# Kernel tuning notes

Measured on AMD Instinct MI355X. Metric: run time of the kernel, lower is better.

The kernel has to match this reference:

```python
import jax, jax.numpy as jnp
import numpy as np

B = 8192        # batch
F = 16          # num_fields
V = 50000       # vocab per field
D = 32          # embed_dim (all equal per assert)
NE = 3          # number of embedding spaces
NL = 3          # cross-net layers
EOD = F * D     # 512 = embed_output_dim
M1, M2, M3 = 512, 256, 128
REG_WEIGHT = 0.01


def setup_inputs() -> dict:
    key = jax.random.key(0)
    ks = jax.random.split(key, 12)
    x = jax.random.randint(ks[0], (B, F), 0, V)
    emb_tables = jax.random.normal(ks[1], (NE, F * V, D), dtype=jnp.float32) * 0.05
    cross_W = jax.random.normal(ks[2], (NE, NL, EOD, EOD), dtype=jnp.float32) * (1.0 / np.sqrt(EOD))
    cross_b = jnp.zeros((NE, NL, EOD), dtype=jnp.float32)
    mlp1_W = jax.random.normal(ks[3], (NE, EOD, M1), dtype=jnp.float32) * (1.0 / np.sqrt(EOD))
    mlp1_b = jnp.zeros((NE, M1), dtype=jnp.float32)
    mlp_W1 = jax.random.normal(ks[4], (M1, M2), dtype=jnp.float32) * (1.0 / np.sqrt(M1))
    mlp_b1 = jnp.zeros((M2,), dtype=jnp.float32)
    mlp_W2 = jax.random.normal(ks[5], (M2, M3), dtype=jnp.float32) * (1.0 / np.sqrt(M2))
    mlp_b2 = jnp.zeros((M3,), dtype=jnp.float32)
    mlp_W3 = jax.random.normal(ks[6], (M3, 1), dtype=jnp.float32) * (1.0 / np.sqrt(M3))
    mlp_b3 = jnp.zeros((1,), dtype=jnp.float32)
    return {"x": x, "emb_tables": emb_tables, "cross_W": cross_W, "cross_b": cross_b,
            "mlp1_W": mlp1_W, "mlp1_b": mlp1_b, "mlp_W1": mlp_W1, "mlp_b1": mlp_b1,
            "mlp_W2": mlp_W2, "mlp_b2": mlp_b2, "mlp_W3": mlp_W3, "mlp_b3": mlp_b3}


def _branch(x0, Ws, bs, W1, b1):
    # DCNv2 cross network: x_{l+1} = x0 * (W_l x_l + b_l) + x_l, then one MLP layer (ReLU)
    xl = x0
    for l in range(NL):
        xl = x0 * (xl @ Ws[l] + bs[l]) + xl
    return jax.nn.relu(xl @ W1 + b1)


def reference(x, emb_tables, cross_W, cross_b, mlp1_W, mlp1_b,
              mlp_W1, mlp_b1, mlp_W2, mlp_b2, mlp_W3, mlp_b3):
    offsets = jnp.arange(F, dtype=x.dtype) * V
    idx = x + offsets                      # [B, F] indices into shared table
    es = emb_tables[:, idx]                # [NE, B, F, D]
    es_flat = es.reshape(NE, B, EOD)       # [NE, B, F*D]
    h = jax.vmap(_branch)(es_flat, cross_W, cross_b, mlp1_W, mlp1_b)  # [NE, B, M1]
    h = h.mean(axis=0)                     # mean over embedding spaces
    h = jax.nn.relu(h @ mlp_W1 + mlp_b1)
    h = jax.nn.relu(h @ mlp_W2 + mlp_b2)
    p = h @ mlp_W3 + mlp_b3                # [B, 1]
    output = jax.nn.sigmoid(p[:, 0])
    # training-path regularizer: per-field cross-embedding Gram SVDs
    pairs = [(1, 0), (2, 0), (2, 1)]
    sims = []
    for i, j in pairs:
        m = jnp.einsum('bkd,bke->kde', es[i], es[j])     # [F, D, D]
        s = jnp.linalg.svd(m, compute_uv=False)          # batched singular values [F, D]
        sims.append(s.mean(axis=0))                      # [D]
    sim = jnp.concatenate(sims)                          # [len(pairs)*D]
    reg_loss = REG_WEIGHT * jnp.mean(sim ** 2)
    return output, reg_loss
```

## Files before the change

### kernel.cpp

```cpp
#include <hip/hip_runtime.h>
#include <math.h>

#define B_ 8192
#define F_ 16
#define V_ 50000
#define D_ 32
#define NE_ 3
#define EOD_ 512
#define M1_ 512
#define M2_ 256
#define M3_ 128
#define BE_ ((size_t)B_ * EOD_)

typedef __attribute__((ext_vector_type(8))) short short8;
typedef __attribute__((ext_vector_type(4))) float floatx4;

__device__ __forceinline__ unsigned short f2bf(float f) {
    union { float f; unsigned u; } v; v.f = f;
    unsigned r = v.u + 0x7FFF + ((v.u >> 16) & 1);
    return (unsigned short)(r >> 16);
}
__device__ __forceinline__ float bf2f(unsigned short h) {
    union { unsigned u; float f; } v; v.u = (unsigned)h << 16;
    return v.f;
}
__device__ __forceinline__ void gld16(const void* g, void* l) {
    __builtin_amdgcn_global_load_lds(
        (const __attribute__((address_space(1))) unsigned int*)g,
        (__attribute__((address_space(3))) unsigned int*)l, 16, 0, 0);
}

__global__ __launch_bounds__(256) void gather_k(const int* __restrict__ x,
    const float* __restrict__ tables, unsigned short* __restrict__ esb)
{
    int gid = blockIdx.x * 256 + threadIdx.x;
    int d8 = gid & 3;
    int f  = (gid >> 2) & 15;
    int b  = (gid >> 6) & (B_ - 1);
    int e  = gid >> 19;
    int idx = x[b * F_ + f] + f * V_;
    const float4* src = (const float4*)(tables + ((size_t)e * F_ * V_ + idx) * D_) + d8 * 2;
    float4 v0 = src[0], v1 = src[1];
    unsigned short o[8];
    o[0] = f2bf(v0.x); o[1] = f2bf(v0.y); o[2] = f2bf(v0.z); o[3] = f2bf(v0.w);
    o[4] = f2bf(v1.x); o[5] = f2bf(v1.y); o[6] = f2bf(v1.z); o[7] = f2bf(v1.w);
    unsigned short* dst = esb + ((size_t)e * B_ + b) * EOD_ + f * D_ + d8 * 8;
    *(uint4*)dst = *(uint4*)o;
}

__global__ __launch_bounds__(256) void wtrans12_k(const float* __restrict__ crossW,
    const float* __restrict__ mlp1W, unsigned short* __restrict__ Wt)
{
    __shared__ float tile[32][33];
    int bn = blockIdx.x * 32, bk = blockIdx.y * 32;
    int mat = blockIdx.z;
    const float* Wm = (mat < 9) ? crossW + (size_t)mat * 512 * 512
                                : mlp1W + (size_t)(mat - 9) * 512 * 512;
    unsigned short* Wtm = Wt + (size_t)mat * 512 * 512;
    int tx = threadIdx.x & 31, ty = threadIdx.x >> 5;
    #pragma unroll
    for (int i = 0; i < 32; i += 8)
        tile[ty + i][tx] = Wm[(size_t)(bk + ty + i) * 512 + bn + tx];
    __syncthreads();
    #pragma unroll
    for (int i = 0; i < 32; i += 8)
        Wtm[(size_t)(bn + ty + i) * 512 + bk + tx] = f2bf(tile[tx][ty + i]);
}

__global__ __launch_bounds__(256) void wtrans_k(const float* __restrict__ W,
    unsigned short* __restrict__ Wt, int K, int N)
{
    __shared__ float tile[32][33];
    int bn = blockIdx.x * 32, bk = blockIdx.y * 32;
    int tx = threadIdx.x & 31, ty = threadIdx.x >> 5;
    #pragma unroll
    for (int i = 0; i < 32; i += 8)
        tile[ty + i][tx] = W[(size_t)(bk + ty + i) * N + bn + tx];
    __syncthreads();
    #pragma unroll
    for (int i = 0; i < 32; i += 8)
        Wt[(size_t)(bn + ty + i) * K + bk + tx] = f2bf(tile[tx][ty + i]);
}

__global__ __launch_bounds__(256) void gemm_mfma_k(
    const unsigned short* __restrict__ A,  long sA,
    const unsigned short* __restrict__ Wt, long sW,
    const float* __restrict__ bias,        long sB,
    const unsigned short* __restrict__ x0, long sX,
    const unsigned short* __restrict__ xl, long sXl,
    unsigned short* __restrict__ outb,     long sO,
    int M, int N, int K, int mode)
{
    int e = blockIdx.z;
    A    += (size_t)e * sA;
    Wt   += (size_t)e * sW;
    bias += (size_t)e * sB;
    outb += (size_t)e * sO;
    if (mode == 0) { x0 += (size_t)e * sX; xl += (size_t)e * sXl; }

    __shared__ unsigned short As[128 * 32];
    __shared__ unsigned short Bs[128 * 32];
    int t = threadIdx.x;
    int w = t >> 6, lane = t & 63;
    int quad = lane >> 4, lid = lane & 15;
    int wr = (w & 1) * 64, wc = (w >> 1) * 64;
    int rowbase = blockIdx.y * 128, colbase = blockIdx.x * 128;

    int chunk = w * 2;
    int sub = lane >> 2;
    int kk = (lane & 3) * 8;
    const unsigned short* pa0 = A  + (size_t)(rowbase + chunk * 16 + sub) * K + kk;
    const unsigned short* pa1 = pa0 + (size_t)16 * K;
    const unsigned short* pb0 = Wt + (size_t)(colbase + chunk * 16 + sub) * K + kk;
    const unsigned short* pb1 = pb0 + (size_t)16 * K;
    unsigned short* la0 = As + chunk * 512 + lane * 8;
    unsigned short* la1 = la0 + 512;
    unsigned short* lb0 = Bs + chunk * 512 + lane * 8;
    unsigned short* lb1 = lb0 + 512;

    floatx4 acc[4][4];
    #pragma unroll
    for (int i = 0; i < 4; i++)
        #pragma unroll
        for (int j = 0; j < 4; j++) acc[i][j] = {0.f, 0.f, 0.f, 0.f};

    for (int k0 = 0; k0 < K; k0 += 32) {
        if (k0) __syncthreads();
        gld16(pa0 + k0, la0);
        gld16(pa1 + k0, la1);
        gld16(pb0 + k0, lb0);
        gld16(pb1 + k0, lb1);
        __syncthreads();
        short8 af[4], bfr[4];
        #pragma unroll
        for (int i = 0; i < 4; i++) {
            af[i]  = *(const short8*)(As + (wr + i * 16 + lid) * 32 + quad * 8);
            bfr[i] = *(const short8*)(Bs + (wc + i * 16 + lid) * 32 + quad * 8);
        }
        #pragma unroll
        for (int i = 0; i < 4; i++)
            #pragma unroll
            for (int j = 0; j < 4; j++)
                acc[i][j] = __builtin_amdgcn_mfma_f32_16x16x32_bf16(af[i], bfr[j], acc[i][j], 0, 0, 0);
    }

    #pragma unroll
    for (int i = 0; i < 4; i++) {
        int row0 = rowbase + wr + i * 16 + quad * 4;
        #pragma unroll
        for (int j = 0; j < 4; j++) {
            int col = colbase + wc + j * 16 + lid;
            float bv = bias[col];
            #pragma unroll
            for (int rr = 0; rr < 4; rr++) {
                size_t off = (size_t)(row0 + rr) * N + col;
                float v = acc[i][j][rr] + bv;
                if (mode == 0)      v = bf2f(x0[off]) * v + bf2f(xl[off]);
                else if (mode == 1) v = fmaxf(v, 0.f) * (1.f / 3.f);
                else                v = fmaxf(v, 0.f);
                outb[off] = f2bf(v);
            }
        }
    }
}

__global__ __launch_bounds__(256) void sum3_k(const unsigned short* __restrict__ h,
                                              unsigned short* __restrict__ o)
{
    size_t i = ((size_t)blockIdx.x * 256 + threadIdx.x) * 8;
    uint4 a = *(const uint4*)(h + i);
    uint4 b = *(const uint4*)(h + BE_ + i);
    uint4 c = *(const uint4*)(h + 2 * BE_ + i);
    const unsigned short* pa = (const unsigned short*)&a;
    const unsigned short* pb = (const unsigned short*)&b;
    const unsigned short* pc = (const unsigned short*)&c;
    unsigned short r[8];
    #pragma unroll
    for (int j = 0; j < 8; j++) r[j] = f2bf(bf2f(pa[j]) + bf2f(pb[j]) + bf2f(pc[j]));
    *(uint4*)(o + i) = *(uint4*)r;
}

__global__ __launch_bounds__(256) void final_k(const unsigned short* __restrict__ h2,
    const float* __restrict__ W3, const float* __restrict__ b3,
    float* __restrict__ out)
{
    int gt = blockIdx.x * 256 + threadIdx.x;
    int s = gt >> 6, lane = gt & 63;
    float p = bf2f(h2[(size_t)s * 128 + lane]) * W3[lane]
            + bf2f(h2[(size_t)s * 128 + 64 + lane]) * W3[64 + lane];
    #pragma unroll
    for (int off = 32; off > 0; off >>= 1) p += __shfl_down(p, off);
    if (lane == 0) out[s] = 1.0f / (1.0f + expf(-(p + b3[0])));
}

__global__ __launch_bounds__(256) void pairsum_k(const unsigned short* __restrict__ es,
                                                 float* __restrict__ m)
{
    const int pi[3] = {1, 2, 2};
    const int pj[3] = {0, 0, 1};
    int pk = blockIdx.x;
    int pair = pk >> 4, k = pk & 15;
    const unsigned short* Ei = es + (size_t)pi[pair] * BE_ + k * D_;
    const unsigned short* Ej = es + (size_t)pj[pair] * BE_ + k * D_;
    int b0 = blockIdx.y * (B_ / 16);

    __shared__ float sa[8][32], sb[8][32];
    int t = threadIdx.x;
    int d = t >> 3, e4 = (t & 7) * 4;
    int lr = t >> 5, lc = t & 31;
    float a0 = 0, a1 = 0, a2 = 0, a3 = 0;

    for (int bb = b0; bb < b0 + B_ / 16; bb += 8) {
        __syncthreads();
        sa[lr][lc] = bf2f(Ei[(size_t)(bb + lr) * EOD_ + lc]);
        sb[lr][lc] = bf2f(Ej[(size_t)(bb + lr) * EOD_ + lc]);
        __syncthreads();
        #pragma unroll
        for (int s2 = 0; s2 < 8; s2++) {
            float avv = sa[s2][d];
            float4 bvv = *(const float4*)&sb[s2][e4];
            a0 += avv * bvv.x; a1 += avv * bvv.y;
            a2 += avv * bvv.z; a3 += avv * bvv.w;
        }
    }
    float* dst = m + (size_t)pk * 1024 + d * 32 + e4;
    atomicAdd(dst + 0, a0); atomicAdd(dst + 1, a1);
    atomicAdd(dst + 2, a2); atomicAdd(dst + 3, a3);
}

__global__ __launch_bounds__(64) void svd_k(const float* __restrict__ mg,
                                            float* __restrict__ sv)
{
    int mat = blockIdx.x;
    int l = threadIdx.x;
    int col = l & 31, half = l >> 5;
    const float* src = mg + (size_t)mat * 1024 + half * 16 * 32 + col;
    float a[16];
    #pragma unroll
    for (int j = 0; j < 16; j++) a[j] = src[j * 32];

    for (int sweep = 0; sweep < 6; sweep++) {
        for (int r = 0; r < 31; r++) {
            int partner, isp;
            if (col == 31) { partner = r; isp = 1; }
            else {
                int u = col - r; if (u < 0) u += 31;
                if (u == 0) { partner = 31; isp = 0; }
                else {
                    int v = 2 * r - col; v %= 31; if (v < 0) v += 31;
                    partner = v;
                    isp = (u <= 15) ? 1 : 0;
                }
            }
            int plane = half * 32 + partner;
            float b[16];
            #pragma unroll
            for (int j = 0; j < 16; j++) b[j] = __shfl(a[j], plane, 64);
            float own = 0.f, cross = 0.f, par = 0.f;
            #pragma unroll
            for (int j = 0; j < 16; j++) {
                own   += a[j] * a[j];
                cross += a[j] * b[j];
                par   += b[j] * b[j];
            }
            own   += __shfl_xor(own, 32);
            cross += __shfl_xor(cross, 32);
            par   += __shfl_xor(par, 32);
            float app = isp ? own : par;
            float aqq = isp ? par : own;
            float c = 1.f, s = 0.f;
            if (fabsf(cross) > 1e-12f) {
                float tau = (aqq - app) / (2.f * cross);
                float tt = (tau >= 0.f) ? 1.f / (tau + sqrtf(1.f + tau * tau))
                                        : 1.f / (tau - sqrtf(1.f + tau * tau));
                c = rsqrtf(1.f + tt * tt); s = tt * c;
            }
            float sgn = isp ? -s : s;
            #pragma unroll
            for (int j = 0; j < 16; j++) a[j] = c * a[j] + sgn * b[j];
        }
    }

    float nn = 0.f;
    #pragma unroll
    for (int j = 0; j < 16; j++) nn += a[j] * a[j];
    nn += __shfl_xor(nn, 32);
    float v = sqrtf(nn);

    __shared__ float ev[32];
    if (half == 0) ev[col] = v;
    if (half == 0) {
        int rank = 0;
        for (int o2 = 0; o2 < 32; o2++) {
            float w = ev[o2];
            if (w > v || (w == v && o2 < col)) rank++;
        }
        sv[(size_t)mat * 32 + rank] = v;
    }
}

__global__ __launch_bounds__(128) void reg_k(const float* __restrict__ sv,
                                             float* __restrict__ out)
{
    __shared__ float red[128];
    int t = threadIdx.x;
    float val = 0.f;
    if (t < 96) {
        int p = t >> 5, d = t & 31;
        float s = 0;
        #pragma unroll
        for (int k = 0; k < 16; k++) s += sv[(size_t)(p * 16 + k) * 32 + d];
        s *= (1.f / 16.f);
        val = s * s;
    }
    red[t] = val; __syncthreads();
    for (int off = 64; off > 0; off >>= 1) {
        if (t < off) red[t] += red[t + off];
        __syncthreads();
    }
    if (t == 0) out[B_] = 0.01f * red[0] / 96.f;
}

extern "C" void kernel_launch(void* const* d_in, const int* in_sizes, int n_in,
                              void* d_out, int out_size, void* d_ws, size_t ws_size,
                              hipStream_t stream)
{
    const int*   x      = (const int*)d_in[0];
    const float* emb    = (const float*)d_in[1];
    const float* crossW = (const float*)d_in[2];
    const float* crossb = (const float*)d_in[3];
    const float* mlp1W  = (const float*)d_in[4];
    const float* mlp1b  = (const float*)d_in[5];
    const float* W1     = (const float*)d_in[6];
    const float* b1     = (const float*)d_in[7];
    const float* W2     = (const float*)d_in[8];
    const float* b2     = (const float*)d_in[9];
    const float* W3     = (const float*)d_in[10];
    const float* b3     = (const float*)d_in[11];
    float* out = (float*)d_out;

    unsigned char* wsb = (unsigned char*)d_ws;
    size_t o = 0;
    auto alloc = [&](size_t bytes) -> void* {
        void* p = wsb + o; o += (bytes + 255) & ~(size_t)255; return p;
    };
    unsigned short* esb  = (unsigned short*)alloc(3 * BE_ * 2);
    unsigned short* B0   = (unsigned short*)alloc(3 * BE_ * 2);
    unsigned short* B1   = (unsigned short*)alloc(3 * BE_ * 2);
    unsigned short* WtC  = (unsigned short*)alloc((size_t)12 * 512 * 512 * 2);
    unsigned short* Wt1  = (unsigned short*)alloc((size_t)512 * 256 * 2);
    unsigned short* Wt2  = (unsigned short*)alloc((size_t)256 * 128 * 2);
    float*          mbuf = (float*)alloc(48 * 1024 * 4);
    float*          svb  = (float*)alloc(48 * 32 * 4);
    unsigned short* WtM  = WtC + (size_t)9 * 512 * 512;
    unsigned short* hsb = B0;
    unsigned short* h1b = B0 + (size_t)B_ * M1_;
    unsigned short* h2b = h1b + (size_t)B_ * M2_;

    wtrans12_k<<<dim3(16, 16, 12), 256, 0, stream>>>(crossW, mlp1W, WtC);
    wtrans_k<<<dim3( 8, 16), 256, 0, stream>>>(W1, Wt1, 512, 256);
    wtrans_k<<<dim3( 4,  8), 256, 0, stream>>>(W2, Wt2, 256, 128);

    gather_k<<<(NE_ * B_ * F_ * 4) / 256, 256, 0, stream>>>(x, emb, esb);

    hipMemsetAsync(mbuf, 0, 48 * 1024 * 4, stream);
    pairsum_k<<<dim3(48, 16), 256, 0, stream>>>(esb, mbuf);
    svd_k<<<48, 64, 0, stream>>>(mbuf, svb);
    reg_k<<<1, 128, 0, stream>>>(svb, out);

    const long sW512 = 3 * 512 * 512;
    gemm_mfma_k<<<dim3(4, 64, 3), 256, 0, stream>>>(
        esb, (long)BE_, WtC, sW512, crossb, 3 * 512,
        esb, (long)BE_, esb, (long)BE_, B0, (long)BE_, B_, EOD_, EOD_, 0);
    gemm_mfma_k<<<dim3(4, 64, 3), 256, 0, stream>>>(
        B0, (long)BE_, WtC + 512 * 512, sW512, crossb + 512, 3 * 512,
        esb, (long)BE_, B0, (long)BE_, B1, (long)BE_, B_, EOD_, EOD_, 0);
    gemm_mfma_k<<<dim3(4, 64, 3), 256, 0, stream>>>(
        B1, (long)BE_, WtC + 2 * 512 * 512, sW512, crossb + 1024, 3 * 512,
        esb, (long)BE_, B1, (long)BE_, B0, (long)BE_, B_, EOD_, EOD_, 0);
    gemm_mfma_k<<<dim3(4, 64, 3), 256, 0, stream>>>(
        B0, (long)BE_, WtM, 512 * 512, mlp1b, 512,
        nullptr, 0, nullptr, 0, B1, (long)BE_, B_, M1_, EOD_, 1);
    sum3_k<<<(B_ * M1_) / (256 * 8), 256, 0, stream>>>(B1, hsb);
    gemm_mfma_k<<<dim3(2, 64, 1), 256, 0, stream>>>(
        hsb, 0, Wt1, 0, b1, 0, nullptr, 0, nullptr, 0,
        h1b, 0, B_, M2_, M1_, 2);
    gemm_mfma_k<<<dim3(1, 64, 1), 256, 0, stream>>>(
        h1b, 0, Wt2, 0, b2, 0, nullptr, 0, nullptr, 0,
        h2b, 0, B_, M3_, M2_, 2);
    final_k<<<(B_ * 64) / 256, 256, 0, stream>>>(h2b, W3, b3, out);
}
```

Before: 704.0 us.

## Fuse cross-network layers and first MLP into one LDS-resident branch kernel

```diff
diff --git a/kernel.cpp b/kernel.cpp
--- a/kernel.cpp
+++ b/kernel.cpp
@@ -82,22 +82,161 @@
         Wt[(size_t)(bn + ty + i) * K + bk + tx] = f2bf(tile[tx][ty + i]);
 }
 
+__global__ __launch_bounds__(256, 1) void branch_k(
+    const unsigned short* __restrict__ es,
+    const unsigned short* __restrict__ Wall,
+    const float* __restrict__ crossb,
+    const float* __restrict__ mlp1b,
+    unsigned short* __restrict__ outp)
+{
+    extern __shared__ unsigned short lds[];
+    unsigned short* xs  = lds;
+    unsigned short* Wst = lds + 32768;
+
+    const int t = threadIdx.x;
+    const int w = t >> 6, lane = t & 63;
+    const int quad = lane >> 4, lid = lane & 15;
+    const int wrow = (w & 1) * 32, wcol = (w >> 1) * 256;
+    const int e = blockIdx.y;
+    const int rowbase = blockIdx.x * 64;
+    const unsigned short* x0g = es + (size_t)e * BE_ + (size_t)rowbase * 512;
+
+    #pragma unroll
+    for (int g = 0; g < 16; g++) {
+        int u = w * 16 + g, c = u >> 2, rb = u & 3;
+        gld16(x0g + (size_t)(rb * 16 + (lane >> 2)) * 512 + c * 32 + (lane & 3) * 8,
+              xs + c * 2048 + rb * 512 + lane * 8);
+    }
+
+    unsigned x0p[2][16][2];
+    float xlf[2][16][4];
+    #pragma unroll
+    for (int i = 0; i < 2; i++)
+        #pragma unroll
+        for (int j = 0; j < 16; j++) {
+            int col = wcol + j * 16 + lid;
+            int r0 = wrow + i * 16 + quad * 4;
+            unsigned short v0 = x0g[(size_t)(r0 + 0) * 512 + col];
+            unsigned short v1 = x0g[(size_t)(r0 + 1) * 512 + col];
+            unsigned short v2 = x0g[(size_t)(r0 + 2) * 512 + col];
+            unsigned short v3 = x0g[(size_t)(r0 + 3) * 512 + col];
+            x0p[i][j][0] = (unsigned)v0 | ((unsigned)v1 << 16);
+            x0p[i][j][1] = (unsigned)v2 | ((unsigned)v3 << 16);
+            xlf[i][j][0] = bf2f(v0); xlf[i][j][1] = bf2f(v1);
+            xlf[i][j][2] = bf2f(v2); xlf[i][j][3] = bf2f(v3);
+        }
+
+    floatx4 acc[2][16];
+
+    for (int l = 0; l < 3; l++) {
+        const unsigned short* Wg = Wall + (size_t)(e * 3 + l) * 262144;
+        const float* bp = crossb + ((size_t)e * 3 + l) * 512;
+        float bv[16];
+        #pragma unroll
+        for (int j = 0; j < 16; j++) bv[j] = bp[wcol + j * 16 + lid];
+        #pragma unroll
+        for (int i = 0; i < 2; i++)
+            #pragma unroll
+            for (int j = 0; j < 16; j++) acc[i][j] = {0.f, 0.f, 0.f, 0.f};
+
+        for (int k0 = 0; k0 < 512; k0 += 32) {
+            __syncthreads();
+            #pragma unroll
+            for (int g = 0; g < 8; g++) {
+                int rb = w * 8 + g;
+                gld16(Wg + (size_t)(rb * 16 + (lane >> 2)) * 512 + k0 + (lane & 3) * 8,
+                      Wst + rb * 512 + lane * 8);
+            }
+            __syncthreads();
+            int c = k0 >> 5;
+            short8 af0 = *(const short8*)(xs + c * 2048 + (wrow + 0 + lid) * 32 + quad * 8);
+            short8 af1 = *(const short8*)(xs + c * 2048 + (wrow + 16 + lid) * 32 + quad * 8);
+            #pragma unroll
+            for (int j = 0; j < 16; j++) {
+                short8 bfv = *(const short8*)(Wst + (wcol + j * 16 + lid) * 32 + quad * 8);
+                acc[0][j] = __builtin_amdgcn_mfma_f32_16x16x32_bf16(af0, bfv, acc[0][j], 0, 0, 0);
+                acc[1][j] = __builtin_amdgcn_mfma_f32_16x16x32_bf16(af1, bfv, acc[1][j], 0, 0, 0);
+            }
+        }
+        __syncthreads();
+
+        #pragma unroll
+        for (int i = 0; i < 2; i++)
+            #pragma unroll
+            for (int j = 0; j < 16; j++) {
+                int col = wcol + j * 16 + lid;
+                int cbase = (col >> 5) * 2048 + (col & 31);
+                int r0 = wrow + i * 16 + quad * 4;
+                #pragma unroll
+                for (int rr = 0; rr < 4; rr++) {
+                    float x0v = bf2f((unsigned short)((x0p[i][j][rr >> 1] >> ((rr & 1) * 16)) & 0xFFFF));
+                    float nv = x0v * (acc[i][j][rr] + bv[j]) + xlf[i][j][rr];
+                    xlf[i][j][rr] = nv;
+                    xs[cbase + (r0 + rr) * 32] = f2bf(nv);
+                }
+            }
+    }
+
+    {
+        const unsigned short* Wg = Wall + (size_t)(9 + e) * 262144;
+        const float* bp = mlp1b + (size_t)e * 512;
+        float bv[16];
+        #pragma unroll
+        for (int j = 0; j < 16; j++) bv[j] = bp[wcol + j * 16 + lid];
+        #pragma unroll
+        for (int i = 0; i < 2; i++)
+            #pragma unroll
+            for (int j = 0; j < 16; j++) acc[i][j] = {0.f, 0.f, 0.f, 0.f};
+
+        for (int k0 = 0; k0 < 512; k0 += 32) {
+            __syncthreads();
+            #pragma unroll
+            for (int g = 0; g < 8; g++) {
+                int rb = w * 8 + g;
+                gld16(Wg + (size_t)(rb * 16 + (lane >> 2)) * 512 + k0 + (lane & 3) * 8,
+                      Wst + rb * 512 + lane * 8);
+            }
+            __syncthreads();
+            int c = k0 >> 5;
+            short8 af0 = *(const short8*)(xs + c * 2048 + (wrow + 0 + lid) * 32 + quad * 8);
+            short8 af1 = *(const short8*)(xs + c * 2048 + (wrow + 16 + lid) * 32 + quad * 8);
+            #pragma unroll
+            for (int j = 0; j < 16; j++) {
+                short8 bfv = *(const short8*)(Wst + (wcol + j * 16 + lid) * 32 + quad * 8);
+                acc[0][j] = __builtin_amdgcn_mfma_f32_16x16x32_bf16(af0, bfv, acc[0][j], 0, 0, 0);
+                acc[1][j] = __builtin_amdgcn_mfma_f32_16x16x32_bf16(af1, bfv, acc[1][j], 0, 0, 0);
+            }
+        }
+        __syncthreads();
+        #pragma unroll
+        for (int i = 0; i < 2; i++)
+            #pragma unroll
+            for (int j = 0; j < 16; j++) {
+                int col = wcol + j * 16 + lid;
+                int r0 = wrow + i * 16 + quad * 4;
+                #pragma unroll
+                for (int rr = 0; rr < 4; rr++) {
+                    float v = fmaxf(acc[i][j][rr] + bv[j], 0.f) * (1.f / 3.f);
+                    xs[(r0 + rr) * 512 + col] = f2bf(v);
+                }
+            }
+        __syncthreads();
+        unsigned short* dst = outp + (size_t)e * BE_ + (size_t)rowbase * 512;
+        #pragma unroll
+        for (int g = 0; g < 16; g++) {
+            int u = g * 256 + t;
+            *(uint4*)(dst + u * 8) = *(const uint4*)(xs + u * 8);
+        }
+    }
+}
+
 __global__ __launch_bounds__(256) void gemm_mfma_k(
-    const unsigned short* __restrict__ A,  long sA,
-    const unsigned short* __restrict__ Wt, long sW,
-    const float* __restrict__ bias,        long sB,
-    const unsigned short* __restrict__ x0, long sX,
-    const unsigned short* __restrict__ xl, long sXl,
-    unsigned short* __restrict__ outb,     long sO,
-    int M, int N, int K, int mode)
-{
-    int e = blockIdx.z;
-    A    += (size_t)e * sA;
-    Wt   += (size_t)e * sW;
-    bias += (size_t)e * sB;
-    outb += (size_t)e * sO;
-    if (mode == 0) { x0 += (size_t)e * sX; xl += (size_t)e * sXl; }
-
+    const unsigned short* __restrict__ A,
+    const unsigned short* __restrict__ Wt,
+    const float* __restrict__ bias,
+    unsigned short* __restrict__ outb,
+    int M, int N, int K)
+{
     __shared__ unsigned short As[128 * 32];
     __shared__ unsigned short Bs[128 * 32];
     int t = threadIdx.x;
@@ -154,11 +293,7 @@
             #pragma unroll
             for (int rr = 0; rr < 4; rr++) {
                 size_t off = (size_t)(row0 + rr) * N + col;
-                float v = acc[i][j][rr] + bv;
-                if (mode == 0)      v = bf2f(x0[off]) * v + bf2f(xl[off]);
-                else if (mode == 1) v = fmaxf(v, 0.f) * (1.f / 3.f);
-                else                v = fmaxf(v, 0.f);
-                outb[off] = f2bf(v);
+                outb[off] = f2bf(fmaxf(acc[i][j][rr] + bv, 0.f));
             }
         }
     }
@@ -352,7 +487,6 @@
     unsigned short* Wt2  = (unsigned short*)alloc((size_t)256 * 128 * 2);
     float*          mbuf = (float*)alloc(48 * 1024 * 4);
     float*          svb  = (float*)alloc(48 * 32 * 4);
-    unsigned short* WtM  = WtC + (size_t)9 * 512 * 512;
     unsigned short* hsb = B0;
     unsigned short* h1b = B0 + (size_t)B_ * M1_;
     unsigned short* h2b = h1b + (size_t)B_ * M2_;
@@ -368,25 +502,9 @@
     svd_k<<<48, 64, 0, stream>>>(mbuf, svb);
     reg_k<<<1, 128, 0, stream>>>(svb, out);
 
-    const long sW512 = 3 * 512 * 512;
-    gemm_mfma_k<<<dim3(4, 64, 3), 256, 0, stream>>>(
-        esb, (long)BE_, WtC, sW512, crossb, 3 * 512,
-        esb, (long)BE_, esb, (long)BE_, B0, (long)BE_, B_, EOD_, EOD_, 0);
-    gemm_mfma_k<<<dim3(4, 64, 3), 256, 0, stream>>>(
-        B0, (long)BE_, WtC + 512 * 512, sW512, crossb + 512, 3 * 512,
-        esb, (long)BE_, B0, (long)BE_, B1, (long)BE_, B_, EOD_, EOD_, 0);
-    gemm_mfma_k<<<dim3(4, 64, 3), 256, 0, stream>>>(
-        B1, (long)BE_, WtC + 2 * 512 * 512, sW512, crossb + 1024, 3 * 512,
-        esb, (long)BE_, B1, (long)BE_, B0, (long)BE_, B_, EOD_, EOD_, 0);
-    gemm_mfma_k<<<dim3(4, 64, 3), 256, 0, stream>>>(
-        B0, (long)BE_, WtM, 512 * 512, mlp1b, 512,
-        nullptr, 0, nullptr, 0, B1, (long)BE_, B_, M1_, EOD_, 1);
+    branch_k<<<dim3(128, 3), 256, 98304, stream>>>(esb, WtC, crossb, mlp1b, B1);
     sum3_k<<<(B_ * M1_) / (256 * 8), 256, 0, stream>>>(B1, hsb);
-    gemm_mfma_k<<<dim3(2, 64, 1), 256, 0, stream>>>(
-        hsb, 0, Wt1, 0, b1, 0, nullptr, 0, nullptr, 0,
-        h1b, 0, B_, M2_, M1_, 2);
-    gemm_mfma_k<<<dim3(1, 64, 1), 256, 0, stream>>>(
-        h1b, 0, Wt2, 0, b2, 0, nullptr, 0, nullptr, 0,
-        h2b, 0, B_, M3_, M2_, 2);
+    gemm_mfma_k<<<dim3(2, 64), 256, 0, stream>>>(hsb, Wt1, b1, h1b, B_, M2_, M1_);
+    gemm_mfma_k<<<dim3(1, 64), 256, 0, stream>>>(h1b, Wt2, b2, h2b, B_, M3_, M2_);
     final_k<<<(B_ * 64) / 256, 256, 0, stream>>>(h2b, W3, b3, out);
 }
```

New measurement: 762.8 us. 1.08x slower.
